# Performance work log

Measured on AMD Instinct MI355X. Metric: run time of the kernel, lower is better.

The kernel has to match this reference:

```python
import jax, jax.numpy as jnp
import numpy as np

N = 50000      # nodes
E = 800000     # edges per metapath
M = 3          # metapaths
H = 2          # heads
IN = 128       # in_dim
HID = 64       # hidden
HEAD = HID // H
OUT = 16       # classes
ATT = 128      # atten_dim


def setup_inputs() -> dict:
    key = jax.random.key(0)
    ks = jax.random.split(key, 12)
    s = 0.05
    return {
        "x": jax.random.normal(ks[0], (N, IN), jnp.float32),
        "edge_index": jax.random.randint(ks[1], (M, 2, E), 0, N, dtype=jnp.int64),
        # per-(metapath, head) GCN params
        "W_enc": jax.random.normal(ks[2], (M, H, IN, HID), jnp.float32) * s,
        "b_enc": jnp.zeros((M, H, HID), jnp.float32),
        "W_conv": jax.random.normal(ks[3], (M, H, HID, HID), jnp.float32) * s,
        "b_conv": jnp.zeros((M, H, HID), jnp.float32),
        "W_dec": jax.random.normal(ks[4], (M, H, HID, HEAD), jnp.float32) * s,
        "b_dec": jnp.zeros((M, H, HEAD), jnp.float32),
        # semantic attention params
        "W_s": jax.random.normal(ks[5], (HID, ATT), jnp.float32) * s,
        "b_s": jnp.zeros((ATT,), jnp.float32),
        "q": jax.random.normal(ks[6], (ATT,), jnp.float32) * s,
        # output projection
        "W_o": jax.random.normal(ks[7], (HID, OUT), jnp.float32) * s,
        "b_o": jnp.zeros((OUT,), jnp.float32),
    }


def _lrelu(v, slope=0.1):
    return jnp.where(v > 0, v, slope * v)


def reference(x, edge_index, W_enc, b_enc, W_conv, b_conv, W_dec, b_dec, W_s, b_s, q, W_o, b_o):
    # encoder for all (metapath, head) at once: [M,H,N,HID]
    h = _lrelu(jnp.einsum('ni,mhio->mhno', x, W_enc) + b_enc[:, :, None, :])

    z_list = []
    for m in range(M):  # small fixed number of metapaths
        src = edge_index[m, 0]
        dst = edge_index[m, 1]
        # GCNConv with self-loops + symmetric normalization (PyG semantics)
        deg = jax.ops.segment_sum(jnp.ones(E, jnp.float32), dst, num_segments=N) + 1.0
        inv_sqrt = jax.lax.rsqrt(deg)
        coef = inv_sqrt[src] * inv_sqrt[dst]                 # [E]
        xw = jnp.einsum('hnd,hdo->hno', h[m], W_conv[m])     # [H,N,HID]
        msg = xw[:, src, :] * coef[None, :, None]            # [H,E,HID] gather
        agg = jax.vmap(lambda mm: jax.ops.segment_sum(mm, dst, num_segments=N))(msg)
        agg = agg + xw * (1.0 / deg)[None, :, None]          # self-loop term (norm = 1/deg)
        agg = agg + b_conv[m][:, None, :]
        hh = _lrelu(agg)
        dec = jnp.einsum('hnd,hdo->hno', hh, W_dec[m]) + b_dec[m][:, None, :]  # [H,N,HEAD]
        z_list.append(jnp.transpose(dec, (1, 0, 2)).reshape(N, HID))           # head concat

    zs = jnp.stack(z_list)                                   # [M,N,HID]
    # semantic attention over metapaths
    hs = jnp.tanh(jnp.einsum('mnd,da->mna', zs, W_s) + b_s)
    beta = jax.nn.softmax(jnp.einsum('mna,a->mn', hs, q).mean(axis=1))  # [M]
    Z = jnp.einsum('m,mnd->nd', beta, zs)                    # [N,HID]
    out = jax.nn.log_softmax(Z @ W_o + b_o, axis=-1)         # [N,OUT]
    return out, beta
```

## Files before the change

kernel.cpp:

```cpp
#include <hip/hip_runtime.h>

#define NN 50000
#define EE 800000
#define MM 3
#define HH 2
#define IND 128
#define HIDD 64
#define HEADD 32
#define OUTD 16
#define ATTD 128

#define NBKT 64
#define BSZ 782

#define NG4 200000
#define BBLK 196
#define QCAP 13200

#define GLS 136
#define XWN 50048

typedef unsigned char u8;
typedef unsigned short u16;
typedef unsigned long long u64;
typedef short bf16x8 __attribute__((ext_vector_type(8)));
typedef unsigned short u16x8 __attribute__((ext_vector_type(8)));
typedef u64 u64x2 __attribute__((ext_vector_type(2)));
typedef unsigned int u32x4 __attribute__((ext_vector_type(4)));
typedef float f32x2 __attribute__((ext_vector_type(2)));
typedef float f32x4 __attribute__((ext_vector_type(4)));

__device__ __forceinline__ float lrelu(float v) { return v > 0.f ? v : 0.1f * v; }

__device__ __forceinline__ float fast_tanh(float x) {
    float ax = fabsf(x);
    float e = __expf(-2.0f * ax);
    float t = (1.0f - e) * __builtin_amdgcn_rcpf(1.0f + e);
    return copysignf(t, x);
}

__device__ __forceinline__ u16 f2b(float f) {
    union { float f; unsigned int u; } v; v.f = f;
    unsigned int r = v.u + 0x7fffu + ((v.u >> 16) & 1u);
    return (u16)(r >> 16);
}
__device__ __forceinline__ float b2f(u16 u) {
    union { unsigned int u; float f; } v; v.u = ((unsigned int)u) << 16; return v.f;
}

__device__ __forceinline__ u8 f2e4hw(float f) {
    int r = __builtin_amdgcn_cvt_pk_fp8_f32(f, f, 0, false);
    return (u8)(r & 0xff);
}

__device__ __forceinline__ void acc16(f32x2* acc, u32x4 w) {
#pragma unroll
    for (int i = 0; i < 4; i++) {
        acc[2 * i]     += __builtin_amdgcn_cvt_pk_f32_fp8(w[i], false);
        acc[2 * i + 1] += __builtin_amdgcn_cvt_pk_f32_fp8(w[i], true);
    }
}

__global__ __launch_bounds__(256) void k_bucket(const int* __restrict__ ei,
                                                u64* __restrict__ queues,
                                                int* __restrict__ gcur) {
    __shared__ int cnt[NBKT];
    __shared__ int base[NBKT];
    const int m = blockIdx.y, tid = threadIdx.x;
    const int4* s4 = (const int4*)(ei + (size_t)m * 2 * EE);
    const int4* d4 = (const int4*)(ei + (size_t)m * 2 * EE + EE);
    const int q0 = blockIdx.x * 1024;
    if (tid < NBKT) cnt[tid] = 0;
    __syncthreads();
#pragma unroll
    for (int i = 0; i < 4; i++) {
        int q = q0 + i * 256 + tid;
        if (q < NG4) {
            int4 v = d4[q];
            atomicAdd(&cnt[v.x / BSZ], 1);
            atomicAdd(&cnt[v.y / BSZ], 1);
            atomicAdd(&cnt[v.z / BSZ], 1);
            atomicAdd(&cnt[v.w / BSZ], 1);
        }
    }
    __syncthreads();
    if (tid < NBKT) { base[tid] = atomicAdd(&gcur[m * NBKT + tid], cnt[tid]); cnt[tid] = 0; }
    __syncthreads();
#pragma unroll
    for (int i = 0; i < 4; i++) {
        int q = q0 + i * 256 + tid;
        if (q < NG4) {
            int4 dv = d4[q];
            int4 sv = s4[q];
            int ds[4] = {dv.x, dv.y, dv.z, dv.w};
            int ss[4] = {sv.x, sv.y, sv.z, sv.w};
#pragma unroll
            for (int e = 0; e < 4; e++) {
                int b = ds[e] / BSZ;
                int slot = base[b] + atomicAdd(&cnt[b], 1);
                if (slot < QCAP) {
                    u64 pk = ((u64)(unsigned)ds[e] << 32) | (unsigned)ss[e];
                    queues[((size_t)(m * NBKT + b)) * QCAP + slot] = pk;
                }
            }
        }
    }
}

__global__ void k_pscan(const int* __restrict__ gcur, int* __restrict__ pbase) {
    int t = threadIdx.x;
    if (t < MM) {
        int run = 0;
        for (int b = 0; b < NBKT; b++) {
            int L = gcur[t * NBKT + b]; if (L > QCAP) L = QCAP;
            pbase[t * NBKT + b] = run; run += L;
        }
    }
}

__global__ __launch_bounds__(512) void k_csr(const u64* __restrict__ queues,
                                             const int* __restrict__ gcur,
                                             const int* __restrict__ pbase,
                                             int* __restrict__ ofs,
                                             float* __restrict__ rs,
                                             int* __restrict__ sorted) {
    __shared__ int cnt[BSZ];
    __shared__ int wscan[8];
    const int m = blockIdx.y;
    const int b = blockIdx.x;
    const int tid = threadIdx.x;
    const int lane = tid & 63, w = tid >> 6;
    int qlen = gcur[m * NBKT + b]; if (qlen > QCAP) qlen = QCAP;
    const u64* q = queues + ((size_t)(m * NBKT + b)) * QCAP;
    const u64x2* q2 = (const u64x2*)q;
    const int dlo = b * BSZ;
    const int nd = min(dlo + BSZ, NN) - dlo;
    const int n2 = qlen >> 1;
    for (int i = tid; i < BSZ; i += 512) cnt[i] = 0;
    __syncthreads();
    for (int i = tid; i < n2; i += 512) {
        u64x2 e = q2[i];
        atomicAdd(&cnt[(int)(e.x >> 32) - dlo], 1);
        atomicAdd(&cnt[(int)(e.y >> 32) - dlo], 1);
    }
    if (tid == 0 && (qlen & 1))
        atomicAdd(&cnt[(int)(q[qlen - 1] >> 32) - dlo], 1);
    __syncthreads();
    const int c0 = tid * 2;
    int v0 = (c0 < BSZ) ? cnt[c0] : 0;
    int v1 = (c0 + 1 < BSZ) ? cnt[c0 + 1] : 0;
    int s = v0 + v1;
    int vv = s;
    for (int off = 1; off < 64; off <<= 1) { int t = __shfl_up(vv, off); if (lane >= off) vv += t; }
    if (lane == 63) wscan[w] = vv;
    __syncthreads();
    if (tid == 0) { int run = 0; for (int j = 0; j < 8; j++) { int t = wscan[j]; wscan[j] = run; run += t; } }
    __syncthreads();
    int excl = wscan[w] + vv - s;
    int g0 = pbase[m * NBKT + b] + excl;
    int g1 = g0 + v0;
    if (c0 < nd) {
        ofs[(size_t)m * (NN + 1) + dlo + c0] = g0;
        rs[(size_t)m * NN + dlo + c0] = rsqrtf((float)(v0 + 1));
    }
    if (c0 + 1 < nd) {
        ofs[(size_t)m * (NN + 1) + dlo + c0 + 1] = g1;
        rs[(size_t)m * NN + dlo + c0 + 1] = rsqrtf((float)(v1 + 1));
    }
    if (b == NBKT - 1 && tid == 0)
        ofs[(size_t)m * (NN + 1) + NN] = EE;
    __syncthreads();
    if (c0 < BSZ) cnt[c0] = g0;
    if (c0 + 1 < BSZ) cnt[c0 + 1] = g1;
    __syncthreads();
    int* srt = sorted + (size_t)m * EE;
    for (int i = tid; i < n2; i += 512) {
        u64x2 e = q2[i];
        int p0 = atomicAdd(&cnt[(int)(e.x >> 32) - dlo], 1);
        srt[p0] = (int)(e.x & 0xffffffffu);
        int p1 = atomicAdd(&cnt[(int)(e.y >> 32) - dlo], 1);
        srt[p1] = (int)(e.y & 0xffffffffu);
    }
    if (tid == 0 && (qlen & 1)) {
        u64 e = q[qlen - 1];
        int p0 = atomicAdd(&cnt[(int)(e >> 32) - dlo], 1);
        srt[p0] = (int)(e & 0xffffffffu);
    }
}

__global__ __launch_bounds__(256) void k_prep(const float* __restrict__ We, const float* __restrict__ Wc,
                                              const float* __restrict__ Wd, const float* __restrict__ Ws,
                                              u16* __restrict__ wbe, u16* __restrict__ wbc,
                                              u16* __restrict__ wbd, u16* __restrict__ wbs) {
    int t = blockIdx.x * 256 + threadIdx.x;
    if (t >= 11776) return;
    bf16x8 val;
    u16* dst;
    if (t < 6144) {
        int m = t >> 11, r = t & 2047;
        int nt = r >> 8, ks = (r >> 6) & 3, lane = r & 63;
        int n = nt * 16 + (lane & 15), h = n >> 6, o = n & 63;
        int kb = ks * 32 + (lane >> 4) * 8;
        const float* w = We + ((size_t)(m * 2 + h) * 128) * 64;
#pragma unroll
        for (int j = 0; j < 8; j++) val[j] = (short)f2b(w[(size_t)(kb + j) * 64 + o]);
        dst = wbe + ((size_t)m * 2048 + r) * 8;
    } else if (t < 9216) {
        int u = t - 6144;
        int m = u >> 10, r = u & 1023;
        int nt = r >> 7, ks = (r >> 6) & 1, lane = r & 63;
        int h = nt >> 2, o = (nt & 3) * 16 + (lane & 15);
        int kb = ks * 32 + (lane >> 4) * 8;
        const float* w = Wc + ((size_t)(m * 2 + h) * 64) * 64;
#pragma unroll
        for (int j = 0; j < 8; j++) val[j] = (short)f2b(w[(size_t)(kb + j) * 64 + o]);
        dst = wbc + ((size_t)m * 1024 + r) * 8;
    } else if (t < 10752) {
        int u = t - 9216;
        int m = u >> 9, r = u & 511;
        int nt = r >> 7, ks = (r >> 6) & 1, lane = r & 63;
        int h = nt >> 1, o = (nt & 1) * 16 + (lane & 15);
        int kb = ks * 32 + (lane >> 4) * 8;
        const float* w = Wd + ((size_t)(m * 2 + h) * 64) * 32;
#pragma unroll
        for (int j = 0; j < 8; j++) val[j] = (short)f2b(w[(size_t)(kb + j) * 32 + o]);
        dst = wbd + ((size_t)m * 512 + r) * 8;
    } else {
        int r = t - 10752;
        int nt = r >> 7, ks = (r >> 6) & 1, lane = r & 63;
        int n = nt * 16 + (lane & 15);
        int kb = ks * 32 + (lane >> 4) * 8;
#pragma unroll
        for (int j = 0; j < 8; j++) val[j] = (short)f2b(Ws[(size_t)(kb + j) * 128 + n]);
        dst = wbs + (size_t)r * 8;
    }
    *(bf16x8*)dst = val;
}

#define HLS 133
__global__ __launch_bounds__(256) void k_encconv(const float* __restrict__ x,
                                                 const u16* __restrict__ wbe_all,
                                                 const float* __restrict__ be_all,
                                                 const u16* __restrict__ wbc_all,
                                                 const float* __restrict__ rs_all,
                                                 u8* __restrict__ xw_all) {
    __shared__ float hl[64 * HLS];
    const int m = blockIdx.y;
    const int tid = threadIdx.x, lane = tid & 63, wave = tid >> 6;
    const int quad = lane >> 4, c16 = lane & 15;
    const int row = blockIdx.x * 64 + wave * 16 + c16;
    const bool ok = row < NN;
    const bf16x8* wbE = (const bf16x8*)(wbe_all + (size_t)m * 2048 * 8);
    const float* be = be_all + m * 2 * 64;
    const float* rs = rs_all + (size_t)m * NN;
    u8* xw = xw_all + (size_t)m * XWN * 128;
    f32x4 zero = {0.f, 0.f, 0.f, 0.f};
    f32x4 acc[8];
#pragma unroll
    for (int nt = 0; nt < 8; nt++) acc[nt] = zero;
#pragma unroll
    for (int ks = 0; ks < 4; ks++) {
        bf16x8 a = {0, 0, 0, 0, 0, 0, 0, 0};
        if (ok) {
            const float* xp = x + (size_t)row * 128 + ks * 32 + quad * 8;
            float4 xa = *(const float4*)xp;
            float4 xb = *(const float4*)(xp + 4);
            a[0] = (short)f2b(xa.x); a[1] = (short)f2b(xa.y);
            a[2] = (short)f2b(xa.z); a[3] = (short)f2b(xa.w);
            a[4] = (short)f2b(xb.x); a[5] = (short)f2b(xb.y);
            a[6] = (short)f2b(xb.z); a[7] = (short)f2b(xb.w);
        }
#pragma unroll
        for (int nt = 0; nt < 8; nt++)
            acc[nt] = __builtin_amdgcn_mfma_f32_16x16x32_bf16(a, wbE[(nt * 4 + ks) * 64 + lane], acc[nt], 0, 0, 0);
    }
    const int rbl = wave * 16 + quad * 4;
#pragma unroll
    for (int nt = 0; nt < 8; nt++) {
        int col = nt * 16 + c16, hh = col >> 6, o = col & 63;
        float bias = be[hh * 64 + o];
#pragma unroll
        for (int j = 0; j < 4; j++) {
            int rl = rbl + j;
            int rg = blockIdx.x * 64 + rl;
            hl[rl * HLS + col] = (rg < NN) ? lrelu(acc[nt][j] + bias) : 0.f;
        }
    }
    __syncthreads();
    const bf16x8* wbC = (const bf16x8*)(wbc_all + (size_t)m * 1024 * 8);
    f32x4 cacc[8];
#pragma unroll
    for (int nt = 0; nt < 8; nt++) cacc[nt] = zero;
    const int rl = wave * 16 + c16;
#pragma unroll
    for (int ks = 0; ks < 2; ks++) {
        bf16x8 a0, a1;
        const float* hp = &hl[rl * HLS + ks * 32 + quad * 8];
#pragma unroll
        for (int j = 0; j < 8; j++) { a0[j] = (short)f2b(hp[j]); a1[j] = (short)f2b(hp[64 + j]); }
#pragma unroll
        for (int nt = 0; nt < 8; nt++)
            cacc[nt] = __builtin_amdgcn_mfma_f32_16x16x32_bf16(nt < 4 ? a0 : a1, wbC[(nt * 2 + ks) * 64 + lane], cacc[nt], 0, 0, 0);
    }
    float rsv[4];
#pragma unroll
    for (int j = 0; j < 4; j++) {
        int r = blockIdx.x * 64 + rbl + j;
        rsv[j] = (r < NN) ? rs[r] * 64.f : 0.f;
    }
#pragma unroll
    for (int nt = 0; nt < 8; nt++) {
        int col = nt * 16 + c16;
#pragma unroll
        for (int j = 0; j < 4; j++) {
            int r = blockIdx.x * 64 + rbl + j;
            xw[(size_t)r * 128 + col] = f2e4hw(cacc[nt][j] * rsv[j]);
        }
    }
}

__global__ __launch_bounds__(512) void k_gpost(const int* __restrict__ sorted_all,
                                               const int* __restrict__ ofs_all,
                                               const float* __restrict__ rs_all,
                                               const u8* __restrict__ xw_all,
                                               const float* __restrict__ bconv_all,
                                               const u16* __restrict__ wbd_all,
                                               const float* __restrict__ bdec_all,
                                               const u16* __restrict__ wbs,
                                               const float* __restrict__ bs,
                                               const float* __restrict__ qv,
                                               u16* __restrict__ z_all,
                                               float* __restrict__ score) {
    __shared__ u16 shm[64 * GLS];
    __shared__ float spart[8];
    u16* ggl = shm;
    float* zl = (float*)shm;
    const int m = blockIdx.y;
    const int tid = threadIdx.x, lane = tid & 63, wave = tid >> 6;
    const int* sorted = sorted_all + (size_t)m * EE;
    const int* ofs = ofs_all + (size_t)m * (NN + 1);
    const float* rs = rs_all + (size_t)m * NN;
    const u8* xw = xw_all + (size_t)m * XWN * 128;
    const float* bconv = bconv_all + m * 2 * 64;
    const float* bdec = bdec_all + m * 2 * 32;
    u16* z = z_all + (size_t)m * NN * 64;

    {
        const int g = lane >> 3, c = lane & 7;
        const int wbase = blockIdx.x * 64 + wave * 8;
        const int dst = wbase + g;
        int ov = 0;
        { int ii = wbase + lane; if (lane < 9) ov = ofs[ii > NN ? NN : ii]; }
        const int beg = __shfl(ov, g);
        const int deg = __shfl(ov, g + 1) - beg;
        int degmax = max(deg, __shfl_xor(deg, 8));
        degmax = max(degmax, __shfl_xor(degmax, 16));
        degmax = max(degmax, __shfl_xor(degmax, 32));
        const int coff = c * 16;

        auto lidx = [&](int j) -> int {
            int t = j + (c & 3);
            return (t < deg) ? sorted[beg + t] : NN;
        };
        auto lrow = [&](int iv, u32x4* wv) {
#pragma unroll
            for (int k = 0; k < 4; k++) {
                int s = __shfl(iv, (lane & 0x38) + k);
                wv[k] = *(const u32x4*)&xw[(size_t)(unsigned)s * 128 + coff];
            }
        };

        f32x2 acc[8];
#pragma unroll
        for (int i = 0; i < 8; i++) acc[i] = 0.f;

        int i0 = lidx(0);
        int i1 = lidx(4);
        {
            int sd = dst < NN ? dst : NN;
            u32x4 w = *(const u32x4*)&xw[(size_t)sd * 128 + coff];
            acc16(acc, w);
        }
        u32x4 wA[4], wB[4];
        lrow(i0, wA);
        const int nch = ((degmax + 7) >> 3) * 2;
        for (int ch = 0; ch < nch; ch += 2) {
            lrow(i1, wB);
            i0 = lidx(ch * 4 + 8);
#pragma unroll
            for (int k = 0; k < 4; k++) acc16(acc, wA[k]);
            lrow(i0, wA);
            i1 = lidx(ch * 4 + 12);
#pragma unroll
            for (int k = 0; k < 4; k++) acc16(acc, wB[k]);
        }

        float rsv = (dst < NN) ? rs[dst] * (1.f / 64.f) : 0.f;
        u16x8 o0, o1;
#pragma unroll
        for (int i = 0; i < 4; i++) {
            o0[2 * i]     = f2b(acc[i].x * rsv);
            o0[2 * i + 1] = f2b(acc[i].y * rsv);
            o1[2 * i]     = f2b(acc[i + 4].x * rsv);
            o1[2 * i + 1] = f2b(acc[i + 4].y * rsv);
        }
        u16* gp = &ggl[(wave * 8 + g) * GLS + coff];
        *(u16x8*)gp = o0;
        *(u16x8*)(gp + 8) = o1;
    }
    __syncthreads();

    f32x4 zero = {0.f, 0.f, 0.f, 0.f};
    const int quad = lane >> 4, c16 = lane & 15;
    const int wq = wave & 3, hi = wave >> 2;
    const int rl = wq * 16 + c16;
    const bf16x8* wd = (const bf16x8*)(wbd_all + (size_t)m * 512 * 8);
    f32x4 pacc[2];
    pacc[0] = zero; pacc[1] = zero;
#pragma unroll
    for (int ks = 0; ks < 2; ks++) {
        bf16x8 a;
        int k0 = ks * 32 + quad * 8;
        const u16* gp = &ggl[rl * GLS + hi * 64 + k0];
#pragma unroll
        for (int j = 0; j < 8; j++)
            a[j] = (short)f2b(lrelu(b2f(gp[j]) + bconv[hi * 64 + k0 + j]));
#pragma unroll
        for (int nt2 = 0; nt2 < 2; nt2++) {
            int nt = hi * 2 + nt2;
            pacc[nt2] = __builtin_amdgcn_mfma_f32_16x16x32_bf16(a, wd[(nt * 2 + ks) * 64 + lane], pacc[nt2], 0, 0, 0);
        }
    }
    __syncthreads();
    {
        const int rbl = wq * 16 + quad * 4;
#pragma unroll
        for (int nt2 = 0; nt2 < 2; nt2++) {
            int nt = hi * 2 + nt2;
            int col = nt * 16 + c16, hh = col >> 5, o = col & 31;
            float bias = bdec[hh * 32 + o];
#pragma unroll
            for (int j = 0; j < 4; j++) {
                int rl2 = rbl + j;
                int rg = blockIdx.x * 64 + rl2;
                zl[rl2 * 68 + col] = (rg < NN) ? (pacc[nt2][j] + bias) : 0.f;
            }
        }
    }
    __syncthreads();

    {
        int rl2 = tid >> 3, cq = tid & 7;
        int rg = blockIdx.x * 64 + rl2;
        if (rg < NN) {
#pragma unroll
            for (int i = 0; i < 2; i++) {
                int c4 = (cq * 2 + i) * 4;
                float4 zv = *(const float4*)&zl[rl2 * 68 + c4];
                ushort4 o;
                o.x = f2b(zv.x); o.y = f2b(zv.y); o.z = f2b(zv.z); o.w = f2b(zv.w);
                *(ushort4*)&z[(size_t)rg * 64 + c4] = o;
            }
        }
    }
    float s = 0.f;
    {
        const bf16x8* wsb = (const bf16x8*)wbs;
        f32x4 sa[4];
#pragma unroll
        for (int nt2 = 0; nt2 < 4; nt2++) sa[nt2] = zero;
#pragma unroll
        for (int ks = 0; ks < 2; ks++) {
            bf16x8 a;
            const float* zp = &zl[rl * 68 + ks * 32 + quad * 8];
#pragma unroll
            for (int j = 0; j < 8; j++) a[j] = (short)f2b(zp[j]);
#pragma unroll
            for (int nt2 = 0; nt2 < 4; nt2++) {
                int nt = hi * 4 + nt2;
                sa[nt2] = __builtin_amdgcn_mfma_f32_16x16x32_bf16(a, wsb[(nt * 2 + ks) * 64 + lane], sa[nt2], 0, 0, 0);
            }
        }
        const int rbl = wq * 16 + quad * 4;
#pragma unroll
        for (int nt2 = 0; nt2 < 4; nt2++) {
            int nt = hi * 4 + nt2;
            int col = nt * 16 + c16;
            float qc = qv[col], bb = bs[col];
#pragma unroll
            for (int j = 0; j < 4; j++) {
                int rg = blockIdx.x * 64 + rbl + j;
                if (rg < NN) s += fast_tanh(sa[nt2][j] + bb) * qc;
            }
        }
#pragma unroll
        for (int off = 1; off < 64; off <<= 1) s += __shfl_xor(s, off);
    }
    if (lane == 0) spart[wave] = s;
    __syncthreads();
    if (tid == 0) {
        float t = spart[0] + spart[1] + spart[2] + spart[3]
                + spart[4] + spart[5] + spart[6] + spart[7];
        atomicAdd(&score[m], t);
    }
}

__global__ void k_beta(const float* __restrict__ score, float* __restrict__ beta_ws,
                       float* __restrict__ out) {
    if (threadIdx.x == 0) {
        float s0 = score[0] / (float)NN, s1 = score[1] / (float)NN, s2 = score[2] / (float)NN;
        float mx = fmaxf(s0, fmaxf(s1, s2));
        float e0 = expf(s0 - mx), e1 = expf(s1 - mx), e2 = expf(s2 - mx);
        float inv = 1.f / (e0 + e1 + e2);
        beta_ws[0] = e0 * inv; beta_ws[1] = e1 * inv; beta_ws[2] = e2 * inv;
        out[800000] = e0 * inv; out[800001] = e1 * inv; out[800002] = e2 * inv;
    }
}

__global__ __launch_bounds__(256) void k_out(const u16* __restrict__ z,
                                             const float* __restrict__ beta,
                                             const float* __restrict__ Wo,
                                             const float* __restrict__ bo,
                                             float* __restrict__ out) {
    __shared__ float Zt[64 * 68];
    __shared__ float Wl[64 * 16];
    __shared__ float bl[16];
    const int tid = threadIdx.x, nbase = blockIdx.x * 64;
    float b0 = beta[0], b1 = beta[1], b2 = beta[2];
    for (int qq = tid; qq < 64 * 16; qq += 256) {
        int node = qq >> 4, k4 = qq & 15;
        int ng = nbase + node;
        float4 v = make_float4(0.f, 0.f, 0.f, 0.f);
        if (ng < NN) {
            ushort4 z0 = *(const ushort4*)&z[((size_t)0 * NN + ng) * 64 + k4 * 4];
            ushort4 z1 = *(const ushort4*)&z[((size_t)1 * NN + ng) * 64 + k4 * 4];
            ushort4 z2 = *(const ushort4*)&z[((size_t)2 * NN + ng) * 64 + k4 * 4];
            v.x = b0 * b2f(z0.x) + b1 * b2f(z1.x) + b2 * b2f(z2.x);
            v.y = b0 * b2f(z0.y) + b1 * b2f(z1.y) + b2 * b2f(z2.y);
            v.z = b0 * b2f(z0.z) + b1 * b2f(z1.z) + b2 * b2f(z2.z);
            v.w = b0 * b2f(z0.w) + b1 * b2f(z1.w) + b2 * b2f(z2.w);
        }
        *(float4*)&Zt[node * 68 + k4 * 4] = v;
    }
    for (int qq = tid; qq < 64 * 16 / 4; qq += 256)
        ((float4*)Wl)[qq] = ((const float4*)Wo)[qq];
    if (tid < 16) bl[tid] = bo[tid];
    __syncthreads();

    const int node = tid >> 2, cg = tid & 3;
    float4 a = make_float4(bl[cg * 4 + 0], bl[cg * 4 + 1], bl[cg * 4 + 2], bl[cg * 4 + 3]);
    for (int k = 0; k < 64; k++) {
        float zv = Zt[node * 68 + k];
        float4 w = *(const float4*)&Wl[k * 16 + cg * 4];
        a.x = fmaf(zv, w.x, a.x);
        a.y = fmaf(zv, w.y, a.y);
        a.z = fmaf(zv, w.z, a.z);
        a.w = fmaf(zv, w.w, a.w);
    }
    float mx = fmaxf(fmaxf(a.x, a.y), fmaxf(a.z, a.w));
    mx = fmaxf(mx, __shfl_xor(mx, 1));
    mx = fmaxf(mx, __shfl_xor(mx, 2));
    float sm = expf(a.x - mx) + expf(a.y - mx) + expf(a.z - mx) + expf(a.w - mx);
    sm += __shfl_xor(sm, 1);
    sm += __shfl_xor(sm, 2);
    float lse = mx + logf(sm);
    int ng = nbase + node;
    if (ng < NN) {
        float4 r = make_float4(a.x - lse, a.y - lse, a.z - lse, a.w - lse);
        *(float4*)&out[(size_t)ng * 16 + cg * 4] = r;
    }
}

extern "C" void kernel_launch(void* const* d_in, const int* in_sizes, int n_in,
                              void* d_out, int out_size, void* d_ws, size_t ws_size,
                              hipStream_t stream) {
    const float* x      = (const float*)d_in[0];
    const int*   ei     = (const int*)d_in[1];
    const float* W_enc  = (const float*)d_in[2];
    const float* b_enc  = (const float*)d_in[3];
    const float* W_conv = (const float*)d_in[4];
    const float* b_conv = (const float*)d_in[5];
    const float* W_dec  = (const float*)d_in[6];
    const float* b_dec  = (const float*)d_in[7];
    const float* W_s    = (const float*)d_in[8];
    const float* b_s    = (const float*)d_in[9];
    const float* qv     = (const float*)d_in[10];
    const float* W_o    = (const float*)d_in[11];
    const float* b_o    = (const float*)d_in[12];
    float* out = (float*)d_out;

    char* ws = (char*)d_ws;
    size_t off = 0;
    auto alloc = [&](size_t bytes) -> char* {
        char* p = ws + off;
        off = (off + bytes + 255) & ~(size_t)255;
        return p;
    };
    int*   row_ofs = (int*)alloc((size_t)MM * (NN + 1) * 4);
    float* rs      = (float*)alloc((size_t)MM * NN * 4);
    int*   sorted  = (int*)alloc((size_t)MM * EE * 4);
    u64*   queues  = (u64*)alloc((size_t)MM * NBKT * QCAP * 8);
    int*   gcur    = (int*)alloc((size_t)MM * NBKT * 4);
    int*   pbase   = (int*)alloc((size_t)MM * NBKT * 4);
    float* score   = (float*)alloc(64);
    float* beta_ws = (float*)alloc(64);
    u16*   wbe     = (u16*)alloc((size_t)MM * 2048 * 8 * 2);
    u16*   wbc     = (u16*)alloc((size_t)MM * 1024 * 8 * 2);
    u16*   wbd     = (u16*)alloc((size_t)MM * 512 * 8 * 2);
    u16*   wbs     = (u16*)alloc((size_t)1024 * 8 * 2);
    u8*    xw_buf  = (u8*)alloc((size_t)MM * XWN * 128);
    u16*   z_buf   = (u16*)alloc((size_t)MM * NN * 64 * 2);

    hipMemsetAsync(gcur, 0, (size_t)MM * NBKT * 4, stream);
    hipMemsetAsync(score, 0, 16, stream);

    dim3 gbkt(BBLK, MM);
    dim3 gcsr(NBKT, MM);
    k_bucket<<<gbkt, 256, 0, stream>>>(ei, queues, gcur);
    k_pscan<<<1, 64, 0, stream>>>(gcur, pbase);
    k_csr<<<gcsr, 512, 0, stream>>>(queues, gcur, pbase, row_ofs, rs, sorted);
    k_prep<<<46, 256, 0, stream>>>(W_enc, W_conv, W_dec, W_s, wbe, wbc, wbd, wbs);

    const int GB = (NN + 63) / 64;
    dim3 gmm(GB, MM);
    k_encconv<<<gmm, 256, 0, stream>>>(x, wbe, b_enc, wbc, rs, xw_buf);
    k_gpost<<<gmm, 512, 0, stream>>>(sorted, row_ofs, rs, xw_buf,
                                     b_conv, wbd, b_dec, wbs, b_s, qv,
                                     z_buf, score);
    k_beta<<<1, 64, 0, stream>>>(score, beta_ws, out);
    k_out<<<GB, 256, 0, stream>>>(z_buf, beta_ws, W_o, b_o, out);
}
```

Measured before the change: 248.1 us.

## Pre-convert x to bf16, deepen gather pipeline, vectorize LDS reads

Adds a kernel that converts x to bf16 once, so the encoder, which runs once per metapath, reads half the bytes and skips the conversion. The neighbour gather in k_gpost now keeps four row groups in flight instead of two, with index loads issued one step ahead, to hide more memory latency. LDS reads in the post-processing are vectorized. This costs an extra kernel launch, another x-sized round trip through memory, and more registers in the gather loop, which may lower occupancy.

```diff
diff --git a/kernel.cpp b/kernel.cpp
--- a/kernel.cpp
+++ b/kernel.cpp
@@ -188,6 +188,19 @@
     }
 }
 
+__global__ __launch_bounds__(256) void k_xcvt(const float* __restrict__ x,
+                                              u16* __restrict__ xb) {
+    int t = blockIdx.x * 256 + threadIdx.x;
+    if (t < NN * IND / 8) {
+        const float4* xp = (const float4*)x + (size_t)t * 2;
+        float4 a = xp[0], b = xp[1];
+        u16x8 o;
+        o[0] = f2b(a.x); o[1] = f2b(a.y); o[2] = f2b(a.z); o[3] = f2b(a.w);
+        o[4] = f2b(b.x); o[5] = f2b(b.y); o[6] = f2b(b.z); o[7] = f2b(b.w);
+        *(u16x8*)&xb[(size_t)t * 8] = o;
+    }
+}
+
 __global__ __launch_bounds__(256) void k_prep(const float* __restrict__ We, const float* __restrict__ Wc,
                                               const float* __restrict__ Wd, const float* __restrict__ Ws,
                                               u16* __restrict__ wbe, u16* __restrict__ wbc,
@@ -238,7 +251,7 @@
 }
 
 #define HLS 133
-__global__ __launch_bounds__(256) void k_encconv(const float* __restrict__ x,
+__global__ __launch_bounds__(256) void k_encconv(const u16* __restrict__ xb,
                                                  const u16* __restrict__ wbe_all,
                                                  const float* __restrict__ be_all,
                                                  const u16* __restrict__ wbc_all,
@@ -261,15 +274,7 @@
 #pragma unroll
     for (int ks = 0; ks < 4; ks++) {
         bf16x8 a = {0, 0, 0, 0, 0, 0, 0, 0};
-        if (ok) {
-            const float* xp = x + (size_t)row * 128 + ks * 32 + quad * 8;
-            float4 xa = *(const float4*)xp;
-            float4 xb = *(const float4*)(xp + 4);
-            a[0] = (short)f2b(xa.x); a[1] = (short)f2b(xa.y);
-            a[2] = (short)f2b(xa.z); a[3] = (short)f2b(xa.w);
-            a[4] = (short)f2b(xb.x); a[5] = (short)f2b(xb.y);
-            a[6] = (short)f2b(xb.z); a[7] = (short)f2b(xb.w);
-        }
+        if (ok) a = *(const bf16x8*)&xb[(size_t)row * 128 + ks * 32 + quad * 8];
 #pragma unroll
         for (int nt = 0; nt < 8; nt++)
             acc[nt] = __builtin_amdgcn_mfma_f32_16x16x32_bf16(a, wbE[(nt * 4 + ks) * 64 + lane], acc[nt], 0, 0, 0);
@@ -349,6 +354,7 @@
         const int g = lane >> 3, c = lane & 7;
         const int wbase = blockIdx.x * 64 + wave * 8;
         const int dst = wbase + g;
+        const bool on = dst < NN;
         int ov = 0;
         { int ii = wbase + lane; if (lane < 9) ov = ofs[ii > NN ? NN : ii]; }
         const int beg = __shfl(ov, g);
@@ -374,28 +380,36 @@
 #pragma unroll
         for (int i = 0; i < 8; i++) acc[i] = 0.f;
 
-        int i0 = lidx(0);
-        int i1 = lidx(4);
         {
-            int sd = dst < NN ? dst : NN;
+            int sd = on ? dst : NN;
             u32x4 w = *(const u32x4*)&xw[(size_t)sd * 128 + coff];
             acc16(acc, w);
         }
-        u32x4 wA[4], wB[4];
-        lrow(i0, wA);
-        const int nch = ((degmax + 7) >> 3) * 2;
-        for (int ch = 0; ch < nch; ch += 2) {
-            lrow(i1, wB);
-            i0 = lidx(ch * 4 + 8);
-#pragma unroll
-            for (int k = 0; k < 4; k++) acc16(acc, wA[k]);
-            lrow(i0, wA);
-            i1 = lidx(ch * 4 + 12);
-#pragma unroll
-            for (int k = 0; k < 4; k++) acc16(acc, wB[k]);
-        }
-
-        float rsv = (dst < NN) ? rs[dst] * (1.f / 64.f) : 0.f;
+
+        u32x4 w0[4], w1[4], w2[4], w3[4];
+        int iA0 = lidx(0), iA1 = lidx(4), iA2 = lidx(8), iA3 = lidx(12);
+        lrow(iA0, w0); lrow(iA1, w1); lrow(iA2, w2); lrow(iA3, w3);
+        int iB0 = lidx(16), iB1 = lidx(20), iB2 = lidx(24), iB3 = lidx(28);
+        const int nit = (degmax + 15) >> 4;
+        for (int it = 0; it < nit; it++) {
+            int nb = (it + 2) * 16;
+            int iC0 = lidx(nb), iC1 = lidx(nb + 4), iC2 = lidx(nb + 8), iC3 = lidx(nb + 12);
+#pragma unroll
+            for (int k = 0; k < 4; k++) acc16(acc, w0[k]);
+            lrow(iB0, w0);
+#pragma unroll
+            for (int k = 0; k < 4; k++) acc16(acc, w1[k]);
+            lrow(iB1, w1);
+#pragma unroll
+            for (int k = 0; k < 4; k++) acc16(acc, w2[k]);
+            lrow(iB2, w2);
+#pragma unroll
+            for (int k = 0; k < 4; k++) acc16(acc, w3[k]);
+            lrow(iB3, w3);
+            iB0 = iC0; iB1 = iC1; iB2 = iC2; iB3 = iC3;
+        }
+
+        float rsv = on ? rs[dst] * (1.f / 64.f) : 0.f;
         u16x8 o0, o1;
 #pragma unroll
         for (int i = 0; i < 4; i++) {
@@ -421,10 +435,10 @@
     for (int ks = 0; ks < 2; ks++) {
         bf16x8 a;
         int k0 = ks * 32 + quad * 8;
-        const u16* gp = &ggl[rl * GLS + hi * 64 + k0];
+        u16x8 gv = *(const u16x8*)&ggl[rl * GLS + hi * 64 + k0];
 #pragma unroll
         for (int j = 0; j < 8; j++)
-            a[j] = (short)f2b(lrelu(b2f(gp[j]) + bconv[hi * 64 + k0 + j]));
+            a[j] = (short)f2b(lrelu(b2f(gv[j]) + bconv[hi * 64 + k0 + j]));
 #pragma unroll
         for (int nt2 = 0; nt2 < 2; nt2++) {
             int nt = hi * 2 + nt2;
@@ -473,8 +487,12 @@
         for (int ks = 0; ks < 2; ks++) {
             bf16x8 a;
             const float* zp = &zl[rl * 68 + ks * 32 + quad * 8];
-#pragma unroll
-            for (int j = 0; j < 8; j++) a[j] = (short)f2b(zp[j]);
+            f32x4 z0 = *(const f32x4*)zp;
+            f32x4 z1 = *(const f32x4*)(zp + 4);
+            a[0] = (short)f2b(z0[0]); a[1] = (short)f2b(z0[1]);
+            a[2] = (short)f2b(z0[2]); a[3] = (short)f2b(z0[3]);
+            a[4] = (short)f2b(z1[0]); a[5] = (short)f2b(z1[1]);
+            a[6] = (short)f2b(z1[2]); a[7] = (short)f2b(z1[3]);
 #pragma unroll
             for (int nt2 = 0; nt2 < 4; nt2++) {
                 int nt = hi * 4 + nt2;
@@ -610,6 +628,7 @@
     u16*   wbs     = (u16*)alloc((size_t)1024 * 8 * 2);
     u8*    xw_buf  = (u8*)alloc((size_t)MM * XWN * 128);
     u16*   z_buf   = (u16*)alloc((size_t)MM * NN * 64 * 2);
+    u16*   xb      = (u16*)alloc((size_t)NN * IND * 2);
 
     hipMemsetAsync(gcur, 0, (size_t)MM * NBKT * 4, stream);
     hipMemsetAsync(score, 0, 16, stream);
@@ -619,11 +638,12 @@
     k_bucket<<<gbkt, 256, 0, stream>>>(ei, queues, gcur);
     k_pscan<<<1, 64, 0, stream>>>(gcur, pbase);
     k_csr<<<gcsr, 512, 0, stream>>>(queues, gcur, pbase, row_ofs, rs, sorted);
+    k_xcvt<<<(NN * IND / 8 + 255) / 256, 256, 0, stream>>>(x, xb);
     k_prep<<<46, 256, 0, stream>>>(W_enc, W_conv, W_dec, W_s, wbe, wbc, wbd, wbs);
 
     const int GB = (NN + 63) / 64;
     dim3 gmm(GB, MM);
-    k_encconv<<<gmm, 256, 0, stream>>>(x, wbe, b_enc, wbc, rs, xw_buf);
+    k_encconv<<<gmm, 256, 0, stream>>>(xb, wbe, b_enc, wbc, rs, xw_buf);
     k_gpost<<<gmm, 512, 0, stream>>>(sorted, row_ofs, rs, xw_buf,
                                      b_conv, wbd, b_dec, wbs, b_s, qv,
                                      z_buf, score);
```

Measured after the change: 253.2 us. +2.1%, slower.
